# Kernel tuning notes

Hardware: AMD Instinct MI355X
Metric: run time of the kernel (lower is better)

Reference implementation:

```python
import jax, jax.numpy as jnp
import numpy as np

NUM_CLASSES = 32000
FEAT_DIM = 256
BATCH = 4096
LAMBDA_C = 1.0
CLAMP_MIN = 1e-12
CLAMP_MAX = 1e12


def setup_inputs() -> dict:
    key = jax.random.key(0)
    k1, k2, k3 = jax.random.split(key, 3)
    embeddings = jax.random.normal(k1, (BATCH, FEAT_DIM), dtype=jnp.float32)
    labels = jax.random.randint(k2, (BATCH,), 0, NUM_CLASSES, dtype=jnp.int64)
    centers = jax.random.normal(k3, (NUM_CLASSES, FEAT_DIM), dtype=jnp.float32)
    return {"embeddings": embeddings, "labels": labels, "centers": centers}


def reference(embeddings, labels, centers):
    batch_size = embeddings.shape[0]
    # distmat[b, c] = ||e_b||^2 + ||c_c||^2 - 2 <e_b, c_c>   [B, C]
    e_sq = jnp.sum(embeddings * embeddings, axis=1, keepdims=True)  # [B, 1]
    c_sq = jnp.sum(centers * centers, axis=1)[None, :]              # [1, C]
    distmat = e_sq + c_sq - 2.0 * jnp.einsum('bd,cd->bc', embeddings, centers)
    # mask: one-hot of labels over classes
    classes = jnp.arange(NUM_CLASSES)
    mask = (labels[:, None] == classes[None, :]).astype(distmat.dtype)  # [B, C]
    dist = jnp.clip(distmat * mask, CLAMP_MIN, CLAMP_MAX)
    loss = jnp.sum(dist) / batch_size
    return loss * LAMBDA_C
```

## Files before the change

kernel.cpp:

```cpp
#include <hip/hip_runtime.h>


#define BATCH 4096
#define FEAT_DIM 256
#define NUM_CLASSES 32000

__global__ __launch_bounds__(256) void center_dist_kernel(
    const float* __restrict__ emb,
    const int* __restrict__ labels,
    const float* __restrict__ centers,
    float* __restrict__ partial)
{
    const int gtid = blockIdx.x * blockDim.x + threadIdx.x;
    const int row  = gtid >> 6;
    const int lane = threadIdx.x & 63;
    if (row >= BATCH) return;

    const int lbl = labels[row];

    const float4 e = *reinterpret_cast<const float4*>(emb + (size_t)row * FEAT_DIM + lane * 4);
    const float4 c = *reinterpret_cast<const float4*>(centers + (size_t)lbl * FEAT_DIM + lane * 4);

    const float d0 = e.x - c.x;
    const float d1 = e.y - c.y;
    const float d2 = e.z - c.z;
    const float d3 = e.w - c.w;
    float s = d0 * d0 + d1 * d1 + d2 * d2 + d3 * d3;

    #pragma unroll
    for (int off = 32; off > 0; off >>= 1)
        s += __shfl_down(s, off, 64);

    if (lane == 0) {
        s = fminf(fmaxf(s, 1e-12f), 1e12f);
        partial[row] = s;
    }
}

__global__ __launch_bounds__(256) void reduce_kernel(
    const float* __restrict__ partial,
    float* __restrict__ out)
{
    __shared__ float sm[256];
    float s = 0.0f;
    for (int i = threadIdx.x; i < BATCH; i += 256)
        s += partial[i];
    sm[threadIdx.x] = s;
    __syncthreads();
    #pragma unroll
    for (int off = 128; off > 0; off >>= 1) {
        if (threadIdx.x < off) sm[threadIdx.x] += sm[threadIdx.x + off];
        __syncthreads();
    }
    if (threadIdx.x == 0) {
        out[0] = sm[0] / (float)BATCH + (float)(NUM_CLASSES - 1) * 1e-12f;
    }
}

extern "C" void kernel_launch(void* const* d_in, const int* in_sizes, int n_in,
                              void* d_out, int out_size, void* d_ws, size_t ws_size,
                              hipStream_t stream) {
    const float* emb     = (const float*)d_in[0];
    const int*   labels  = (const int*)d_in[1];
    const float* centers = (const float*)d_in[2];
    float* out     = (float*)d_out;
    float* partial = (float*)d_ws;

    const int threads = 256;
    const int blocks  = (BATCH * 64) / threads;
    center_dist_kernel<<<blocks, threads, 0, stream>>>(emb, labels, centers, partial);
    reduce_kernel<<<1, threads, 0, stream>>>(partial, out);
}
```

Measured before the change: 14.77 us.

## Fuse per-row distance and final reduction into one kernel with atomics

Replaces the two-kernel scheme (per-row distances written to workspace, then a single-block reduce) with one kernel. Each wave handles four rows, and per-block sums are combined with a float atomicAdd into the output, which is zeroed by a memset. This removes the second kernel launch and the serial single-block reduction. In exchange it adds a memset, makes the float summation order nondeterministic, and issues 256 atomics to one address.

```diff
diff --git a/kernel.cpp b/kernel.cpp
--- a/kernel.cpp
+++ b/kernel.cpp
@@ -5,55 +5,42 @@
 #define FEAT_DIM 256
 #define NUM_CLASSES 32000
 
-__global__ __launch_bounds__(256) void center_dist_kernel(
+__global__ __launch_bounds__(256) void center_loss_fused(
     const float* __restrict__ emb,
     const int* __restrict__ labels,
     const float* __restrict__ centers,
-    float* __restrict__ partial)
-{
-    const int gtid = blockIdx.x * blockDim.x + threadIdx.x;
-    const int row  = gtid >> 6;
-    const int lane = threadIdx.x & 63;
-    if (row >= BATCH) return;
-
-    const int lbl = labels[row];
-
-    const float4 e = *reinterpret_cast<const float4*>(emb + (size_t)row * FEAT_DIM + lane * 4);
-    const float4 c = *reinterpret_cast<const float4*>(centers + (size_t)lbl * FEAT_DIM + lane * 4);
-
-    const float d0 = e.x - c.x;
-    const float d1 = e.y - c.y;
-    const float d2 = e.z - c.z;
-    const float d3 = e.w - c.w;
-    float s = d0 * d0 + d1 * d1 + d2 * d2 + d3 * d3;
-
-    #pragma unroll
-    for (int off = 32; off > 0; off >>= 1)
-        s += __shfl_down(s, off, 64);
-
-    if (lane == 0) {
-        s = fminf(fmaxf(s, 1e-12f), 1e12f);
-        partial[row] = s;
-    }
-}
-
-__global__ __launch_bounds__(256) void reduce_kernel(
-    const float* __restrict__ partial,
     float* __restrict__ out)
 {
-    __shared__ float sm[256];
-    float s = 0.0f;
-    for (int i = threadIdx.x; i < BATCH; i += 256)
-        s += partial[i];
-    sm[threadIdx.x] = s;
+    const int wave = threadIdx.x >> 6;
+    const int lane = threadIdx.x & 63;
+    const int rowBase = blockIdx.x * 16 + wave * 4;
+
+    float acc = 0.0f;
+    #pragma unroll
+    for (int r = 0; r < 4; ++r) {
+        const int row = rowBase + r;
+        const int lbl = labels[row];
+        const float4 e = *reinterpret_cast<const float4*>(emb + (size_t)row * FEAT_DIM + lane * 4);
+        const float4 c = *reinterpret_cast<const float4*>(centers + (size_t)lbl * FEAT_DIM + lane * 4);
+        const float d0 = e.x - c.x;
+        const float d1 = e.y - c.y;
+        const float d2 = e.z - c.z;
+        const float d3 = e.w - c.w;
+        float s = d0 * d0 + d1 * d1 + d2 * d2 + d3 * d3;
+        #pragma unroll
+        for (int off = 1; off < 64; off <<= 1)
+            s += __shfl_xor(s, off, 64);
+        acc += fminf(fmaxf(s, 1e-12f), 1e12f);
+    }
+
+    __shared__ float wsum[4];
+    if (lane == 0) wsum[wave] = acc;
     __syncthreads();
-    #pragma unroll
-    for (int off = 128; off > 0; off >>= 1) {
-        if (threadIdx.x < off) sm[threadIdx.x] += sm[threadIdx.x + off];
-        __syncthreads();
-    }
     if (threadIdx.x == 0) {
-        out[0] = sm[0] / (float)BATCH + (float)(NUM_CLASSES - 1) * 1e-12f;
+        float bs = (wsum[0] + wsum[1] + wsum[2] + wsum[3]) * (1.0f / (float)BATCH);
+        if (blockIdx.x == 0)
+            bs += (float)(NUM_CLASSES - 1) * 1e-12f;
+        atomicAdd(out, bs);
     }
 }
 
@@ -63,11 +50,8 @@
     const float* emb     = (const float*)d_in[0];
     const int*   labels  = (const int*)d_in[1];
     const float* centers = (const float*)d_in[2];
-    float* out     = (float*)d_out;
-    float* partial = (float*)d_ws;
+    float* out = (float*)d_out;
 
-    const int threads = 256;
-    const int blocks  = (BATCH * 64) / threads;
-    center_dist_kernel<<<blocks, threads, 0, stream>>>(emb, labels, centers, partial);
-    reduce_kernel<<<1, threads, 0, stream>>>(partial, out);
+    hipMemsetAsync(out, 0, sizeof(float), stream);
+    center_loss_fused<<<256, 256, 0, stream>>>(emb, labels, centers, out);
 }
```

Result: no change. 14.58 us (-1.3%).
